# Performance work log

Hardware: AMD Instinct MI355X
Metric: run time of the kernel (lower is better)

The kernel has to match this reference:

```python
import jax, jax.numpy as jnp
import numpy as np

B, T, D, P, ALPHA, PR = 4, 4096, 1024, 512, 4, 64


def setup_inputs() -> dict:
    key = jax.random.key(0)
    ks = jax.random.split(key, 9)
    g = lambda k, shape, scale: jax.random.normal(k, shape, jnp.float32) * scale
    return {
        "x": jax.random.normal(ks[0], (B, T, D), jnp.float32),
        "W_toP": g(ks[1], (D, P), D ** -0.5),
        "W_U": g(ks[2], (D, P, ALPHA), D ** -0.5),
        "W_F": g(ks[3], (D, P), D ** -0.5),
        "W_V": g(ks[4], (P, ALPHA), 1.0),
        "W_lam": g(ks[5], (P, PR), P ** -0.5),
        "B_mat": g(ks[6], (P, PR), P ** -0.5),
        "C_mat": g(ks[7], (PR, P), PR ** -0.5),
        "W_fromP": g(ks[8], (P, D), P ** -0.5),
    }


def reference(x, W_toP, W_U, W_F, W_V, W_lam, B_mat, C_mat, W_fromP):
    # dense pre-path: (B,T,D)->(B,T,P)
    pre = jnp.einsum('btd,dp->btp', x, W_toP)
    # CeptaEmbedding dense pathway: multi-factor projection U, gates F, weighted Y
    U = jnp.einsum('btd,dpa->btpa', x, W_U)            # (B,T,P,alpha)
    Fg = jax.nn.sigmoid(jnp.einsum('btd,dp->btp', x, W_F))  # (B,T,P) in (0,1)
    Y = U * W_V                                        # (B,T,P,alpha)
    # CeptaRouting(reduce='sum'): sum over alpha factors, plus residual pre-path
    t = Y.sum(-1) + pre                                # (B,T,P)
    # CeptaSSMLowRank: input-dependent diagonal decay in rank-PR state space
    lam = jax.nn.sigmoid(jnp.einsum('btp,pr->btr', Fg, W_lam))  # (B,T,PR)
    u_in = jnp.einsum('btp,pr->btr', t, B_mat)                  # (B,T,PR)

    def step(s, inp):
        l, u = inp
        s = l * s + u
        return s, s

    s0 = jnp.zeros((x.shape[0], PR), x.dtype)
    _, s_seq = jax.lax.scan(step, s0, (lam.transpose(1, 0, 2), u_in.transpose(1, 0, 2)))
    s_seq = s_seq.transpose(1, 0, 2)                   # (B,T,PR)
    t_tilde = t + jnp.einsum('btr,rp->btp', s_seq, C_mat)
    h = jnp.einsum('btp,pd->btd', t_tilde, W_fromP)    # dropout p=0 -> identity
    return h
```

## Files before the change

### kernel.cpp

```cpp
#include <hip/hip_runtime.h>
#include <hip/hip_bf16.h>

#define Bb 4
#define Tt 4096
#define Dd 1024
#define Pp 512
#define PRr 64
#define Mm (Bb*Tt)
#define NCH 256
#define CL  16

typedef __bf16 bf16;
typedef __bf16 bf16x8 __attribute__((ext_vector_type(8)));
typedef __bf16 bf16x4 __attribute__((ext_vector_type(4)));
typedef float f32x4 __attribute__((ext_vector_type(4)));

#define GPTR(p) (const __attribute__((address_space(1))) void*)(p)
#define LPTR(p) (__attribute__((address_space(3))) void*)(p)

__device__ __forceinline__ float sigmoidf_(float x) {
    return 1.0f / (1.0f + __expf(-x));
}


__global__ void prep_all(const float* __restrict__ W_toP, const float* __restrict__ W_U,
                         const float* __restrict__ W_V, const float* __restrict__ W_F,
                         const float* __restrict__ B_mat, const float* __restrict__ W_lam,
                         bf16* __restrict__ W1t, bf16* __restrict__ W3t,
                         float* __restrict__ CW) {
    int bid = blockIdx.x;
    if (bid < 4096) {
        int idx = bid * 256 + threadIdx.x;
        int n = idx >> 10, k = idx & 1023;
        float v;
        if (n < Pp) {
            int p = n;
            float4 u  = *(const float4*)(W_U + ((size_t)k * Pp + p) * 4);
            float4 wv = *(const float4*)(W_V + (size_t)p * 4);
            v = W_toP[(size_t)k * Pp + p] + u.x * wv.x + u.y * wv.y + u.z * wv.z + u.w * wv.w;
        } else {
            v = W_F[(size_t)k * Pp + (n - Pp)];
        }
        W1t[idx] = (bf16)v;
    } else if (bid < 4608) {
        int idx = (bid - 4096) * 256 + threadIdx.x;
        int n = idx >> 10, k = idx & 1023;
        float v = 0.0f;
        if (n < PRr) { if (k < Pp) v = B_mat[(size_t)k * PRr + n]; }
        else         { if (k >= Pp) v = W_lam[(size_t)(k - Pp) * PRr + (n - PRr)]; }
        W3t[idx] = (bf16)v;
    } else {
        int i = (bid - 4608) * 256 + threadIdx.x;
        ((f32x4*)CW)[i] = (f32x4){};
    }
}

__global__ void prep_cw(const float* __restrict__ C_mat, const float* __restrict__ W_fromP,
                        float* __restrict__ CW) {
    __shared__ float crow[64];
    int nc = blockIdx.x;
    int r  = blockIdx.y;
    int pc = blockIdx.z;
    int tid = threadIdx.x;
    if (tid < 64) crow[tid] = C_mat[(size_t)r * Pp + pc * 64 + tid];
    __syncthreads();
    int n = nc * 256 + tid;
    float acc = 0.0f;
    #pragma unroll 8
    for (int i = 0; i < 64; ++i)
        acc = fmaf(crow[i], W_fromP[(size_t)(pc * 64 + i) * Dd + n], acc);
    atomicAdd(&CW[(size_t)r * Dd + n], acc);
}

__global__ void prep_w2(const float* __restrict__ W_fromP, const float* __restrict__ CW,
                        bf16* __restrict__ W2t) {
    int n = blockIdx.x;
    int k = threadIdx.x;
    float v = (k < Pp) ? W_fromP[(size_t)k * Dd + n]
                       : CW[(size_t)(k - Pp) * Dd + n];
    W2t[(size_t)n * 576 + k] = (bf16)v;
}

__global__ void scan_phase1(const float* __restrict__ UL,
                            float* __restrict__ slocal, float* __restrict__ pprod,
                            float* __restrict__ carryS, float* __restrict__ carryP) {
    int b = blockIdx.y;
    int c = blockIdx.x * 4 + (threadIdx.x >> 6);
    int r = threadIdx.x & 63;
    const float* ulb = UL + ((size_t)b * Tt + (size_t)c * CL) * 128;
    float* sl = slocal + ((size_t)b * Tt + (size_t)c * CL) * PRr;
    float* pp = pprod  + ((size_t)b * Tt + (size_t)c * CL) * PRr;
    float uv[CL], lv[CL];
    #pragma unroll
    for (int i = 0; i < CL; i++) {
        uv[i] = ulb[(size_t)i * 128 + r];
        lv[i] = ulb[(size_t)i * 128 + 64 + r];
    }
    float s = 0.0f, p = 1.0f;
    #pragma unroll
    for (int i = 0; i < CL; i++) {
        s = fmaf(lv[i], s, uv[i]);
        p *= lv[i];
        sl[(size_t)i * PRr + r] = s;
        pp[(size_t)i * PRr + r] = p;
    }
    int ci = b * NCH + c;
    carryS[(size_t)ci * PRr + r] = s;
    carryP[(size_t)ci * PRr + r] = p;
}

__global__ void scan_phase2(const float* __restrict__ carryS, const float* __restrict__ carryP,
                            float* __restrict__ carryIn) {
    int b = blockIdx.x, r = threadIdx.x;
    float carry = 0.0f;
    for (int c0 = 0; c0 < NCH; c0 += 16) {
        float cs[16], cp[16];
        #pragma unroll
        for (int i = 0; i < 16; i++) {
            size_t idx = ((size_t)b * NCH + c0 + i) * PRr + r;
            cs[i] = carryS[idx];
            cp[i] = carryP[idx];
        }
        #pragma unroll
        for (int i = 0; i < 16; i++) {
            carryIn[((size_t)b * NCH + c0 + i) * PRr + r] = carry;
            carry = fmaf(cp[i], carry, cs[i]);
        }
    }
}

__global__ void scan_phase3(const float* __restrict__ slocal, const float* __restrict__ pprod,
                            const float* __restrict__ carryIn, bf16* __restrict__ sb) {
    int i = blockIdx.x * 256 + threadIdx.x;
    int r = i & (PRr - 1);
    int row = i >> 6;
    int b = row >> 12;
    int t = row & (Tt - 1);
    int c = t / CL;
    float carry = carryIn[((size_t)b * NCH + c) * PRr + r];
    sb[i] = (bf16)fmaf(pprod[i], carry, slocal[i]);
}

template <int EPI, int AF32>
__global__ __launch_bounds__(512, 2) void gemm256(
    const bf16* __restrict__ A0, int lda0,
    const bf16* __restrict__ A1, int lda1, int ksplit,
    const float* __restrict__ Af,
    const bf16* __restrict__ Bt, int ldb, int K,
    void* __restrict__ Cout, int ldc, int sigcol) {

    __shared__ bf16 As[2][256 * 64];
    __shared__ bf16 Bs[2][256 * 64];

    const int tid  = threadIdx.x;
    const int lane = tid & 63;
    const int wid  = tid >> 6;
    const int wm   = wid >> 2;
    const int wn   = wid & 3;

    const int cpx = gridDim.x >> 3;
    const int bid = blockIdx.x;
    const int swz = (bid & 7) * cpx + (bid >> 3);
    const int mBase = (swz >> 2) * 256;
    const int nBase = (swz & 3) * 256;

    const int lr  = lane & 15;
    const int q16 = (lane >> 4) * 16;

    auto srcA = [&](int kt, const bf16*& src, int& lda, int& kc) {
        if (kt < ksplit) { src = A0; lda = lda0; kc = kt; }
        else             { src = A1; lda = lda1; kc = kt - ksplit; }
    };

    auto stage = [&](const bf16* src, int lda, int kc, int rowBase, bf16* lbuf, int rd) {
        int d = rd * 8192 + tid * 16;
        int L = d ^ (((d >> 7) & 7) << 4);
        int r = L >> 7;
        int c = (L & 127) >> 1;
        const bf16* g = src + (size_t)(rowBase + r) * lda + (kc + c);
        __builtin_amdgcn_global_load_lds(GPTR(g), LPTR((char*)lbuf + d), 16, 0, 0);
    };

    auto frag = [&](const bf16* lbuf, int r, int cb) -> bf16x8 {
        int flat = r * 128 + cb;
        int phys = flat ^ (((flat >> 7) & 7) << 4);
        return *(const bf16x8*)((const char*)lbuf + phys);
    };

    int rrA[4], ccA[4];
    #pragma unroll
    for (int rd = 0; rd < 4; ++rd) {
        int d = rd * 8192 + tid * 16;
        int L = d ^ (((d >> 7) & 7) << 4);
        rrA[rd] = L >> 7;
        ccA[rd] = (L & 127) >> 1;
    }
    f32x4 H0[4], H1[4];

    auto issueH = [&](f32x4 (&v)[4], int kc, int rdb) {
        #pragma unroll
        for (int rd = 0; rd < 2; ++rd) {
            const float* g = Af + (size_t)(mBase + rrA[rdb + rd]) * Dd + kc + ccA[rdb + rd];
            v[2 * rd]     = *(const f32x4*)(g);
            v[2 * rd + 1] = *(const f32x4*)(g + 4);
        }
        asm volatile("" ::: "memory");
    };
    auto writeH = [&](f32x4 (&v)[4], bf16* lbuf, int rdb) {
        #pragma unroll
        for (int rd = 0; rd < 2; ++rd) {
            bf16x8 o;
            #pragma unroll
            for (int j = 0; j < 4; ++j) {
                o[j]     = (bf16)v[2 * rd][j];
                o[j + 4] = (bf16)v[2 * rd + 1][j];
            }
            *(bf16x8*)((char*)lbuf + (rdb + rd) * 8192 + tid * 16) = o;
        }
    };

    const int NT = K / 64;

    if (AF32) {
        issueH(H0, 0, 0); issueH(H1, 0, 2);
        stage(Bt, ldb, 0, nBase, Bs[0], 0); stage(Bt, ldb, 0, nBase, Bs[0], 1);
        stage(Bt, ldb, 0, nBase, Bs[0], 2); stage(Bt, ldb, 0, nBase, Bs[0], 3);
        writeH(H0, As[0], 0);
        writeH(H1, As[0], 2);
        if (NT > 1) { issueH(H0, 64, 0); issueH(H1, 64, 2); }
        asm volatile("s_waitcnt lgkmcnt(0)" ::: "memory");
        if (NT > 1) asm volatile("s_waitcnt vmcnt(8)" ::: "memory");
        else        asm volatile("s_waitcnt vmcnt(0)" ::: "memory");
    } else {
        const bf16* sa; int la, kc; srcA(0, sa, la, kc);
        stage(sa, la, kc, mBase, As[0], 0); stage(sa, la, kc, mBase, As[0], 2);
        stage(Bt, ldb, 0, nBase, Bs[0], 0); stage(Bt, ldb, 0, nBase, Bs[0], 1);
        stage(Bt, ldb, 0, nBase, Bs[0], 2); stage(Bt, ldb, 0, nBase, Bs[0], 3);
        stage(sa, la, kc, mBase, As[0], 1); stage(sa, la, kc, mBase, As[0], 3);
        asm volatile("s_waitcnt vmcnt(2)" ::: "memory");
    }
    __builtin_amdgcn_s_barrier();

    f32x4 acc[8][4] = {};
    bf16x8 a[4], b0[4], b1[4];

#define MFMA16(AOFF, AV, BV)                                                          \
    _Pragma("unroll")                                                                 \
    for (int m_ = 0; m_ < 4; ++m_)                                                    \
        _Pragma("unroll")                                                             \
        for (int n_ = 0; n_ < 4; ++n_)                                                \
            acc[m_ + AOFF][n_] = __builtin_amdgcn_mfma_f32_16x16x32_bf16(             \
                AV[m_], BV[n_], acc[m_ + AOFF][n_], 0, 0, 0);

    if (AF32) {
        for (int t = 0; t < NT; ++t) {
            bf16* Ac = As[t & 1];       bf16* Bc = Bs[t & 1];
            bf16* An = As[(t + 1) & 1]; bf16* Bn = Bs[(t + 1) & 1];
            const bool hn  = (t + 1 < NT);
            const bool hn2 = (t + 2 < NT);
            const int ktn  = (t + 1) * 64;
            const int ktn2 = (t + 2) * 64;

            #pragma unroll
            for (int i = 0; i < 4; ++i) a[i]  = frag(Ac, wm * 128 + i * 16 + lr, q16);
            #pragma unroll
            for (int i = 0; i < 4; ++i) b0[i] = frag(Bc, wn * 64 + i * 16 + lr, q16);
            if (hn) { stage(Bt, ldb, ktn, nBase, Bn, 0); stage(Bt, ldb, ktn, nBase, Bn, 1); }
            __builtin_amdgcn_s_barrier();
            __builtin_amdgcn_s_setprio(1);
            MFMA16(0, a, b0)
            __builtin_amdgcn_s_setprio(0);
            __builtin_amdgcn_s_barrier();

            #pragma unroll
            for (int i = 0; i < 4; ++i) a[i] = frag(Ac, wm * 128 + (i + 4) * 16 + lr, q16);
            if (hn) { stage(Bt, ldb, ktn, nBase, Bn, 2); stage(Bt, ldb, ktn, nBase, Bn, 3); }
            __builtin_amdgcn_s_barrier();
            __builtin_amdgcn_s_setprio(1);
            MFMA16(4, a, b0)
            __builtin_amdgcn_s_setprio(0);
            __builtin_amdgcn_s_barrier();

            #pragma unroll
            for (int i = 0; i < 4; ++i) a[i]  = frag(Ac, wm * 128 + i * 16 + lr, 64 + q16);
            #pragma unroll
            for (int i = 0; i < 4; ++i) b1[i] = frag(Bc, wn * 64 + i * 16 + lr, 64 + q16);
            if (hn)  writeH(H0, An, 0);
            if (hn2) issueH(H0, ktn2, 0);
            if (hn)  asm volatile("s_waitcnt lgkmcnt(0)" ::: "memory");
            __builtin_amdgcn_s_barrier();
            __builtin_amdgcn_s_setprio(1);
            MFMA16(0, a, b1)
            __builtin_amdgcn_s_setprio(0);
            __builtin_amdgcn_s_barrier();

            #pragma unroll
            for (int i = 0; i < 4; ++i) a[i] = frag(Ac, wm * 128 + (i + 4) * 16 + lr, 64 + q16);
            if (hn)  writeH(H1, An, 2);
            if (hn2) issueH(H1, ktn2, 2);
            if (hn)  asm volatile("s_waitcnt lgkmcnt(0)" ::: "memory");
            if (hn2)      asm volatile("s_waitcnt vmcnt(8)" ::: "memory");
            else if (hn)  asm volatile("s_waitcnt vmcnt(0)" ::: "memory");
            __builtin_amdgcn_s_barrier();
            __builtin_amdgcn_s_setprio(1);
            MFMA16(4, a, b1)
            __builtin_amdgcn_s_setprio(0);
            __builtin_amdgcn_s_barrier();
        }
    } else {
        for (int t = 0; t < NT; ++t) {
            bf16* Ac = As[t & 1];       bf16* Bc = Bs[t & 1];
            bf16* An = As[(t + 1) & 1]; bf16* Bn = Bs[(t + 1) & 1];
            const bool hn = (t + 1 < NT);
            const bf16* sa = A0; int la = lda0, kc = 0;
            if (hn) srcA((t + 1) * 64, sa, la, kc);
            const int ktn = (t + 1) * 64;

            #pragma unroll
            for (int i = 0; i < 4; ++i) a[i]  = frag(Ac, wm * 128 + i * 16 + lr, q16);
            #pragma unroll
            for (int i = 0; i < 4; ++i) b0[i] = frag(Bc, wn * 64 + i * 16 + lr, q16);
            if (hn) {
                stage(sa, la, kc, mBase, An, 0); stage(sa, la, kc, mBase, An, 2);
                asm volatile("s_waitcnt vmcnt(2)" ::: "memory");
            } else {
                asm volatile("s_waitcnt vmcnt(0)" ::: "memory");
            }
            __builtin_amdgcn_s_barrier();
            __builtin_amdgcn_s_setprio(1);
            MFMA16(0, a, b0)
            __builtin_amdgcn_s_setprio(0);
            __builtin_amdgcn_s_barrier();

            #pragma unroll
            for (int i = 0; i < 4; ++i) a[i] = frag(Ac, wm * 128 + (i + 4) * 16 + lr, q16);
            if (hn) { stage(Bt, ldb, ktn, nBase, Bn, 0); stage(Bt, ldb, ktn, nBase, Bn, 1); }
            __builtin_amdgcn_s_barrier();
            __builtin_amdgcn_s_setprio(1);
            MFMA16(4, a, b0)
            __builtin_amdgcn_s_setprio(0);
            __builtin_amdgcn_s_barrier();

            #pragma unroll
            for (int i = 0; i < 4; ++i) a[i]  = frag(Ac, wm * 128 + i * 16 + lr, 64 + q16);
            #pragma unroll
            for (int i = 0; i < 4; ++i) b1[i] = frag(Bc, wn * 64 + i * 16 + lr, 64 + q16);
            if (hn) { stage(Bt, ldb, ktn, nBase, Bn, 2); stage(Bt, ldb, ktn, nBase, Bn, 3); }
            __builtin_amdgcn_s_barrier();
            __builtin_amdgcn_s_setprio(1);
            MFMA16(0, a, b1)
            __builtin_amdgcn_s_setprio(0);
            __builtin_amdgcn_s_barrier();

            #pragma unroll
            for (int i = 0; i < 4; ++i) a[i] = frag(Ac, wm * 128 + (i + 4) * 16 + lr, 64 + q16);
            if (hn) {
                stage(sa, la, kc, mBase, An, 1); stage(sa, la, kc, mBase, An, 3);
                asm volatile("s_waitcnt vmcnt(2)" ::: "memory");
            }
            __builtin_amdgcn_s_barrier();
            __builtin_amdgcn_s_setprio(1);
            MFMA16(4, a, b1)
            __builtin_amdgcn_s_setprio(0);
            __builtin_amdgcn_s_barrier();
        }
    }
#undef MFMA16

    const int lr4 = (lane >> 4) * 4;
    #pragma unroll
    for (int m = 0; m < 8; ++m) {
        #pragma unroll
        for (int n = 0; n < 4; ++n) {
            #pragma unroll
            for (int j = 0; j < 4; ++j) {
                int row = mBase + wm * 128 + m * 16 + lr4 + j;
                int col = nBase + wn * 64 + n * 16 + lr;
                float v = acc[m][n][j];
                if (EPI == 0) {
                    if (col >= sigcol) v = sigmoidf_(v);
                    ((bf16*)Cout)[(size_t)row * ldc + col] = (bf16)v;
                } else {
                    ((float*)Cout)[(size_t)row * ldc + col] = v;
                }
            }
        }
    }
}

__global__ __launch_bounds__(256) void gemm_bt64(
    const bf16* __restrict__ A, int lda,
    const bf16* __restrict__ Bt, int K,
    float* __restrict__ Cout, int ldc, int sigcol) {

    __shared__ bf16 As[64][32];
    __shared__ bf16 Bs[128][32];

    const int tid  = threadIdx.x;
    const int lane = tid & 63;
    const int wid  = tid >> 6;
    const int wr   = (wid >> 1) * 32;
    const int wc   = (wid & 1) * 64;
    const int mBase = blockIdx.x * 64;

    f32x4 acc[2][4] = {};

    const int lr = lane & 15;
    const int lk = (lane >> 4) * 8;

    for (int kt = 0; kt < K; kt += 32) {
        __syncthreads();
        {
            int c = tid;
            int row = c >> 2, k8 = (c & 3) * 8;
            const bf16* g = A + (size_t)(mBase + row) * lda + (kt + k8);
            __builtin_amdgcn_global_load_lds(GPTR(g), LPTR(&As[0][0] + c * 8), 16, 0, 0);
        }
        #pragma unroll
        for (int i = 0; i < 2; i++) {
            int c = tid + i * 256;
            int row = c >> 2, k8 = (c & 3) * 8;
            const bf16* g = Bt + (size_t)row * K + (kt + k8);
            __builtin_amdgcn_global_load_lds(GPTR(g), LPTR(&Bs[0][0] + c * 8), 16, 0, 0);
        }
        __syncthreads();

        bf16x8 af[2], bfr[4];
        #pragma unroll
        for (int m = 0; m < 2; m++) af[m]  = *(const bf16x8*)(&As[wr + m * 16 + lr][lk]);
        #pragma unroll
        for (int n = 0; n < 4; n++) bfr[n] = *(const bf16x8*)(&Bs[wc + n * 16 + lr][lk]);
        #pragma unroll
        for (int m = 0; m < 2; m++)
            #pragma unroll
            for (int n = 0; n < 4; n++)
                acc[m][n] = __builtin_amdgcn_mfma_f32_16x16x32_bf16(af[m], bfr[n], acc[m][n], 0, 0, 0);
    }

    const int lr4 = (lane >> 4) * 4;
    const int lc  = lane & 15;
    #pragma unroll
    for (int m = 0; m < 2; m++) {
        #pragma unroll
        for (int n = 0; n < 4; n++) {
            #pragma unroll
            for (int j = 0; j < 4; j++) {
                int row = mBase + wr + m * 16 + lr4 + j;
                int col = wc + n * 16 + lc;
                float v = acc[m][n][j];
                if (col >= sigcol) v = sigmoidf_(v);
                Cout[(size_t)row * ldc + col] = v;
            }
        }
    }
}

extern "C" void kernel_launch(void* const* d_in, const int* in_sizes, int n_in,
                              void* d_out, int out_size, void* d_ws, size_t ws_size,
                              hipStream_t stream) {
    const float* x       = (const float*)d_in[0];
    const float* W_toP   = (const float*)d_in[1];
    const float* W_U     = (const float*)d_in[2];
    const float* W_F     = (const float*)d_in[3];
    const float* W_V     = (const float*)d_in[4];
    const float* W_lam   = (const float*)d_in[5];
    const float* B_mat   = (const float*)d_in[6];
    const float* C_mat   = (const float*)d_in[7];
    const float* W_fromP = (const float*)d_in[8];
    float* out = (float*)d_out;

    char* ws = (char*)d_ws;
    size_t off = 0;
    auto alloc = [&](size_t bytes) { void* p = ws + off; off = (off + bytes + 255) & ~255ULL; return p; };
    bf16*  TF  = (bf16*)alloc((size_t)Mm * 1024 * 2);
    float* UL  = (float*)alloc((size_t)Mm * 128 * 4);
    bf16*  sb  = (bf16*)alloc((size_t)Mm * PRr * 2);
    bf16*  W1t = (bf16*)alloc((size_t)1024 * 1024 * 2);
    bf16*  W3t = (bf16*)alloc((size_t)128 * 1024 * 2);
    bf16*  W2t = (bf16*)alloc((size_t)1024 * 576 * 2);
    float* CW  = (float*)alloc((size_t)PRr * Dd * 4);
    float* slocal = (float*)alloc((size_t)Mm * PRr * 4);
    float* pprod  = (float*)alloc((size_t)Mm * PRr * 4);
    float* carryS = (float*)alloc((size_t)Bb * NCH * PRr * 4);
    float* carryP = (float*)alloc((size_t)Bb * NCH * PRr * 4);
    float* carryI = (float*)alloc((size_t)Bb * NCH * PRr * 4);

    prep_all<<<dim3(4672), dim3(256), 0, stream>>>(W_toP, W_U, W_V, W_F,
                                                   B_mat, W_lam, W1t, W3t, CW);
    prep_cw<<<dim3(4, 64, 8), dim3(256), 0, stream>>>(C_mat, W_fromP, CW);
    prep_w2<<<dim3(1024), dim3(576), 0, stream>>>(W_fromP, CW, W2t);

    gemm256<0, 1><<<dim3((Mm / 256) * (1024 / 256)), 512, 0, stream>>>(
        nullptr, 0, nullptr, 0, 1 << 30, x, W1t, Dd, Dd, TF, 1024, Pp);

    gemm_bt64<<<dim3(Mm / 64), 256, 0, stream>>>(
        TF, 1024, W3t, 1024, UL, 128, PRr);

    scan_phase1<<<dim3(NCH / 4, Bb), dim3(256), 0, stream>>>(UL, slocal, pprod, carryS, carryP);
    scan_phase2<<<dim3(Bb), dim3(PRr), 0, stream>>>(carryS, carryP, carryI);
    scan_phase3<<<dim3(Mm * PRr / 256), dim3(256), 0, stream>>>(slocal, pprod, carryI, sb);

    gemm256<2, 0><<<dim3((Mm / 256) * (1024 / 256)), 512, 0, stream>>>(
        TF, 1024, sb, PRr, Pp, nullptr, W2t, 576, 576, out, Dd, 1 << 30);
}
```

Measured before the change: 137.1 us.

## Fuse three-phase chunked scan into single-pass decoupled-lookback scan kernel

Replaces the three scan kernels (local chunk scan, serial carry propagation, carry application) with one kernel. Each block publishes its 64-step aggregate through global flags and waits on its predecessors' flags before computing its carry-in. Intermediate slocal/pprod buffers and two launches go away, which removes roughly 16 MB of fp32 round-trip traffic. In exchange it relies on inter-block spin-waiting, which assumes all 256 blocks are co-resident or scheduled in order. The flags are reset by an extra block in prep_all.

Result: slower. 153.9 us (+12.2%).

```diff
diff --git a/kernel.cpp b/kernel.cpp
--- a/kernel.cpp
+++ b/kernel.cpp
@@ -27,7 +27,7 @@
                          const float* __restrict__ W_V, const float* __restrict__ W_F,
                          const float* __restrict__ B_mat, const float* __restrict__ W_lam,
                          bf16* __restrict__ W1t, bf16* __restrict__ W3t,
-                         float* __restrict__ CW) {
+                         float* __restrict__ CW, unsigned int* __restrict__ flags) {
     int bid = blockIdx.x;
     if (bid < 4096) {
         int idx = bid * 256 + threadIdx.x;
@@ -49,9 +49,11 @@
         if (n < PRr) { if (k < Pp) v = B_mat[(size_t)k * PRr + n]; }
         else         { if (k >= Pp) v = W_lam[(size_t)(k - Pp) * PRr + (n - PRr)]; }
         W3t[idx] = (bf16)v;
-    } else {
+    } else if (bid < 4672) {
         int i = (bid - 4608) * 256 + threadIdx.x;
         ((f32x4*)CW)[i] = (f32x4){};
+    } else {
+        flags[threadIdx.x] = 0u;
     }
 }
 
@@ -81,64 +83,90 @@
     W2t[(size_t)n * 576 + k] = (bf16)v;
 }
 
-__global__ void scan_phase1(const float* __restrict__ UL,
-                            float* __restrict__ slocal, float* __restrict__ pprod,
-                            float* __restrict__ carryS, float* __restrict__ carryP) {
-    int b = blockIdx.y;
-    int c = blockIdx.x * 4 + (threadIdx.x >> 6);
-    int r = threadIdx.x & 63;
+__global__ void scan_fused(const float* __restrict__ UL,
+                           float* __restrict__ aggS, float* __restrict__ aggP,
+                           unsigned int* __restrict__ flags,
+                           bf16* __restrict__ sb) {
+    int cg = blockIdx.x;
+    int b  = blockIdx.y;
+    int tid = threadIdx.x;
+    int ci = tid >> 6;
+    int r  = tid & 63;
+    int c  = cg * 4 + ci;
     const float* ulb = UL + ((size_t)b * Tt + (size_t)c * CL) * 128;
-    float* sl = slocal + ((size_t)b * Tt + (size_t)c * CL) * PRr;
-    float* pp = pprod  + ((size_t)b * Tt + (size_t)c * CL) * PRr;
+
     float uv[CL], lv[CL];
     #pragma unroll
     for (int i = 0; i < CL; i++) {
         uv[i] = ulb[(size_t)i * 128 + r];
         lv[i] = ulb[(size_t)i * 128 + 64 + r];
     }
+    float sv[CL], pv[CL];
     float s = 0.0f, p = 1.0f;
     #pragma unroll
     for (int i = 0; i < CL; i++) {
         s = fmaf(lv[i], s, uv[i]);
         p *= lv[i];
-        sl[(size_t)i * PRr + r] = s;
-        pp[(size_t)i * PRr + r] = p;
-    }
-    int ci = b * NCH + c;
-    carryS[(size_t)ci * PRr + r] = s;
-    carryP[(size_t)ci * PRr + r] = p;
-}
-
-__global__ void scan_phase2(const float* __restrict__ carryS, const float* __restrict__ carryP,
-                            float* __restrict__ carryIn) {
-    int b = blockIdx.x, r = threadIdx.x;
-    float carry = 0.0f;
-    for (int c0 = 0; c0 < NCH; c0 += 16) {
-        float cs[16], cp[16];
-        #pragma unroll
-        for (int i = 0; i < 16; i++) {
-            size_t idx = ((size_t)b * NCH + c0 + i) * PRr + r;
-            cs[i] = carryS[idx];
-            cp[i] = carryP[idx];
-        }
-        #pragma unroll
-        for (int i = 0; i < 16; i++) {
-            carryIn[((size_t)b * NCH + c0 + i) * PRr + r] = carry;
-            carry = fmaf(cp[i], carry, cs[i]);
-        }
-    }
-}
-
-__global__ void scan_phase3(const float* __restrict__ slocal, const float* __restrict__ pprod,
-                            const float* __restrict__ carryIn, bf16* __restrict__ sb) {
-    int i = blockIdx.x * 256 + threadIdx.x;
-    int r = i & (PRr - 1);
-    int row = i >> 6;
-    int b = row >> 12;
-    int t = row & (Tt - 1);
-    int c = t / CL;
-    float carry = carryIn[((size_t)b * NCH + c) * PRr + r];
-    sb[i] = (bf16)fmaf(pprod[i], carry, slocal[i]);
+        sv[i] = s; pv[i] = p;
+    }
+
+    __shared__ float shS[4][64], shP[4][64];
+    __shared__ float rS[4][64], rP[4][64];
+    __shared__ float shC[64];
+    shS[ci][r] = s; shP[ci][r] = p;
+    __syncthreads();
+
+    float accS = 0.0f, accP = 1.0f, preS = 0.0f, preP = 1.0f;
+    #pragma unroll
+    for (int j = 0; j < 4; j++) {
+        if (j == ci) { preS = accS; preP = accP; }
+        accS = fmaf(shP[j][r], accS, shS[j][r]);
+        accP *= shP[j][r];
+    }
+
+    if (ci == 0) {
+        int slot = (b * 64 + cg) * 64 + r;
+        aggS[slot] = accS;
+        aggP[slot] = accP;
+        __threadfence();
+        if (r == 0)
+            __hip_atomic_store(&flags[b * 64 + cg], 1u,
+                               __ATOMIC_RELEASE, __HIP_MEMORY_SCOPE_AGENT);
+    }
+
+    if (tid < cg) {
+        while (__hip_atomic_load(&flags[b * 64 + tid],
+                                 __ATOMIC_ACQUIRE, __HIP_MEMORY_SCOPE_AGENT) == 0) {}
+    }
+    __syncthreads();
+    __threadfence();
+
+    int w = ci;
+    float wS = 0.0f, wP = 1.0f;
+    int j0 = w * 16;
+    int j1 = j0 + 16 < cg ? j0 + 16 : cg;
+    for (int j = j0; j < j1; ++j) {
+        float Sj = aggS[(b * 64 + j) * 64 + r];
+        float Pj = aggP[(b * 64 + j) * 64 + r];
+        wS = fmaf(Pj, wS, Sj);
+        wP *= Pj;
+    }
+    rS[w][r] = wS; rP[w][r] = wP;
+    __syncthreads();
+    if (ci == 0) {
+        float x = 0.0f;
+        #pragma unroll
+        for (int w2 = 0; w2 < 4; ++w2) x = fmaf(rP[w2][r], x, rS[w2][r]);
+        shC[r] = x;
+    }
+    __syncthreads();
+
+    float x   = shC[r];
+    float cin = fmaf(preP, x, preS);
+    bf16* sbo = sb + ((size_t)b * Tt + (size_t)c * CL) * PRr;
+    #pragma unroll
+    for (int i = 0; i < CL; i++)
+        sbo[(size_t)i * PRr + r] = (bf16)fmaf(pv[i], cin, sv[i]);
 }
 
 template <int EPI, int AF32>
@@ -479,14 +507,12 @@
     bf16*  W3t = (bf16*)alloc((size_t)128 * 1024 * 2);
     bf16*  W2t = (bf16*)alloc((size_t)1024 * 576 * 2);
     float* CW  = (float*)alloc((size_t)PRr * Dd * 4);
-    float* slocal = (float*)alloc((size_t)Mm * PRr * 4);
-    float* pprod  = (float*)alloc((size_t)Mm * PRr * 4);
-    float* carryS = (float*)alloc((size_t)Bb * NCH * PRr * 4);
-    float* carryP = (float*)alloc((size_t)Bb * NCH * PRr * 4);
-    float* carryI = (float*)alloc((size_t)Bb * NCH * PRr * 4);
-
-    prep_all<<<dim3(4672), dim3(256), 0, stream>>>(W_toP, W_U, W_V, W_F,
-                                                   B_mat, W_lam, W1t, W3t, CW);
+    float* aggS = (float*)alloc((size_t)Bb * 64 * PRr * 4);
+    float* aggP = (float*)alloc((size_t)Bb * 64 * PRr * 4);
+    unsigned int* flags = (unsigned int*)alloc((size_t)Bb * 64 * 4);
+
+    prep_all<<<dim3(4673), dim3(256), 0, stream>>>(W_toP, W_U, W_V, W_F,
+                                                   B_mat, W_lam, W1t, W3t, CW, flags);
     prep_cw<<<dim3(4, 64, 8), dim3(256), 0, stream>>>(C_mat, W_fromP, CW);
     prep_w2<<<dim3(1024), dim3(576), 0, stream>>>(W_fromP, CW, W2t);
 
@@ -496,9 +522,7 @@
     gemm_bt64<<<dim3(Mm / 64), 256, 0, stream>>>(
         TF, 1024, W3t, 1024, UL, 128, PRr);
 
-    scan_phase1<<<dim3(NCH / 4, Bb), dim3(256), 0, stream>>>(UL, slocal, pprod, carryS, carryP);
-    scan_phase2<<<dim3(Bb), dim3(PRr), 0, stream>>>(carryS, carryP, carryI);
-    scan_phase3<<<dim3(Mm * PRr / 256), dim3(256), 0, stream>>>(slocal, pprod, carryI, sb);
+    scan_fused<<<dim3(NCH / 4, Bb), dim3(256), 0, stream>>>(UL, aggS, aggP, flags, sb);
 
     gemm256<2, 0><<<dim3((Mm / 256) * (1024 / 256)), 512, 0, stream>>>(
         TF, 1024, sb, PRr, Pp, nullptr, W2t, 576, 576, out, Dd, 1 << 30);
```
